# Kernel tuning notes

Measured on AMD Instinct MI355X. Metric: run time of the kernel, lower is better.

Reference implementation:

```python
import jax, jax.numpy as jnp
import numpy as np

GROUPS = 32
EPS = 1e-5


def _group_norm(x, scale, bias):
    B, C, H, W = x.shape
    xg = x.reshape(B, GROUPS, -1)
    mu = xg.mean(axis=-1, keepdims=True)
    var = jnp.mean(jnp.square(xg - mu), axis=-1, keepdims=True)
    xn = ((xg - mu) * jax.lax.rsqrt(var + EPS)).reshape(B, C, H, W)
    return xn * scale[None, :, None, None] + bias[None, :, None, None]


def _conv1x1(x, w, b):
    # x: [B,C,H,W], w: [O,C], b: [O]
    return jnp.einsum('bchw,oc->bohw', x, w) + b[None, :, None, None]


def setup_inputs() -> dict:
    key = jax.random.key(0)
    ks = jax.random.split(key, 6)
    B, C, H, W = 16, 512, 32, 32
    x = jax.random.normal(ks[0], (B, C, H, W), dtype=jnp.float32)
    # xavier_uniform for [C, C, 1, 1] conv: limit = sqrt(6 / (fan_in + fan_out)) = sqrt(6 / (2C))
    lim = float(np.sqrt(6.0 / (2 * C)))
    wq = jax.random.uniform(ks[1], (C, C), jnp.float32, -lim, lim)
    wk = jax.random.uniform(ks[2], (C, C), jnp.float32, -lim, lim)
    wv = jax.random.uniform(ks[3], (C, C), jnp.float32, -lim, lim)
    wo = jax.random.uniform(ks[4], (C, C), jnp.float32, -lim, lim) * 1e-5  # gain=1e-5
    zeros_c = jnp.zeros((C,), jnp.float32)
    return {
        'x': x,
        'gn_scale': jnp.ones((C,), jnp.float32),
        'gn_bias': zeros_c,
        'wq': wq, 'bq': zeros_c,
        'wk': wk, 'bk': zeros_c,
        'wv': wv, 'bv': zeros_c,
        'wo': wo, 'bo': zeros_c,
    }


def reference(x, gn_scale, gn_bias, wq, bq, wk, bk, wv, bv, wo, bo):
    B, C, H, W = x.shape
    N = H * W
    h = _group_norm(x, gn_scale, gn_bias)
    q = _conv1x1(h, wq, bq).reshape(B, C, N)  # [B,C,N]
    k = _conv1x1(h, wk, bk).reshape(B, C, N)
    v = _conv1x1(h, wv, bv).reshape(B, C, N)
    scale = 1.0 / jnp.sqrt(jnp.asarray(C, x.dtype))
    w = jnp.einsum('bcn,bcm->bnm', q, k) * scale  # [B,N,N]
    w = jax.nn.softmax(w, axis=-1)
    hv = jnp.einsum('bnm,bcm->bcn', w, v).reshape(B, C, H, W)
    out = _conv1x1(hv, wo, bo)
    return x + out
```

## Files before the change

### kernel.cpp

```cpp
#include <hip/hip_runtime.h>
#include <hip/hip_bf16.h>
#include <cstdint>

typedef unsigned char u8;
typedef float floatx4 __attribute__((ext_vector_type(4)));
typedef int intx8 __attribute__((ext_vector_type(8)));

__device__ __forceinline__ void gld_lds16(const void* g, void* l) {
    __builtin_amdgcn_global_load_lds(
        (const __attribute__((address_space(1))) unsigned int*)g,
        (__attribute__((address_space(3))) unsigned int*)l, 16, 0, 0);
}

__device__ __forceinline__ u8 f2fp8(float v) {
    return (u8)(__builtin_amdgcn_cvt_pk_fp8_f32(v, v, 0, false) & 0xff);
}
__device__ __forceinline__ unsigned int pack4_fp8(float a, float b, float c, float d) {
    unsigned int u = __builtin_amdgcn_cvt_pk_fp8_f32(a, b, 0, false);
    u = __builtin_amdgcn_cvt_pk_fp8_f32(c, d, u, true);
    return u;
}

__device__ __forceinline__ intx8 ld_frag(const u8* p, int lo, int hi) {
    uint4 a = *(const uint4*)(p + lo);
    uint4 b = *(const uint4*)(p + hi);
    intx8 r;
    r[0] = a.x; r[1] = a.y; r[2] = a.z; r[3] = a.w;
    r[4] = b.x; r[5] = b.y; r[6] = b.z; r[7] = b.w;
    return r;
}
__device__ __forceinline__ intx8 ld_frag_g(const u8* p) {
    uint4 a = *(const uint4*)(p);
    uint4 b = *(const uint4*)(p + 16);
    intx8 r;
    r[0] = a.x; r[1] = a.y; r[2] = a.z; r[3] = a.w;
    r[4] = b.x; r[5] = b.y; r[6] = b.z; r[7] = b.w;
    return r;
}

__global__ __launch_bounds__(256) void setup_kernel(
    const float* __restrict__ x, const float* __restrict__ gs,
    const float* __restrict__ gb,
    const float* __restrict__ wq, const float* __restrict__ wk,
    const float* __restrict__ wv, const float* __restrict__ wo,
    const float* __restrict__ bq, const float* __restrict__ bk,
    const float* __restrict__ bv,
    u8* __restrict__ hT, u8* __restrict__ wqkv, u8* __restrict__ wob,
    float* __restrict__ bqkv, float* __restrict__ lsum)
{
    const int t = threadIdx.x;
    if (blockIdx.x >= 512) {
        int i = (blockIdx.x - 512) * 256 + t;
        if (i < 786432) {
            int which = i >> 18;
            int off = i & 262143;
            const float* src = which == 0 ? wq : which == 1 ? wk : wv;
            wqkv[i] = f2fp8(src[off]);
        } else {
            wob[i - 786432] = f2fp8(wo[i - 786432] * 262144.0f);
        }
        if (i < 1536)
            bqkv[i] = i < 512 ? bq[i] : (i < 1024 ? bk[i - 512] : bv[i - 1024]);
        if (i < 16384)
            lsum[i] = 0.0f;
        return;
    }
    const int b = blockIdx.x >> 5;
    const int g = blockIdx.x & 31;
    const int wave = t >> 6, lane = t & 63;
    const float4* x4 = (const float4*)(x + ((long long)b * 512 + g * 16) * 1024);

    float4 v[16];
    float s1 = 0.f, s2 = 0.f;
#pragma unroll
    for (int i = 0; i < 16; ++i) {
        v[i] = x4[i * 256 + t];
        s1 += v[i].x + v[i].y + v[i].z + v[i].w;
        s2 += v[i].x * v[i].x + v[i].y * v[i].y + v[i].z * v[i].z + v[i].w * v[i].w;
    }
#pragma unroll
    for (int m = 32; m; m >>= 1) {
        s1 += __shfl_xor(s1, m, 64);
        s2 += __shfl_xor(s2, m, 64);
    }
    __shared__ float red[2][4];
    __shared__ float stats[2];
    if (lane == 0) { red[0][wave] = s1; red[1][wave] = s2; }
    __syncthreads();
    if (t == 0) {
        float a = red[0][0] + red[0][1] + red[0][2] + red[0][3];
        float q = red[1][0] + red[1][1] + red[1][2] + red[1][3];
        float mu = a * (1.0f / 16384.0f);
        float var = q * (1.0f / 16384.0f) - mu * mu;
        stats[0] = mu;
        stats[1] = rsqrtf(var + 1e-5f);
    }
    __syncthreads();
    const float mu = stats[0], rs = stats[1];

#pragma unroll
    for (int i = 0; i < 16; ++i) {
        const float sc = gs[g * 16 + i] * rs;
        const float bi = gb[g * 16 + i] - mu * sc;
        v[i].x = v[i].x * sc + bi;
        v[i].y = v[i].y * sc + bi;
        v[i].z = v[i].z * sc + bi;
        v[i].w = v[i].w * sc + bi;
    }
    u8* hb = hT + (long long)b * 524288 + g * 16;
#pragma unroll
    for (int r = 0; r < 4; ++r) {
        uint4 o;
        o.x = pack4_fp8(v[0][r],  v[1][r],  v[2][r],  v[3][r]);
        o.y = pack4_fp8(v[4][r],  v[5][r],  v[6][r],  v[7][r]);
        o.z = pack4_fp8(v[8][r],  v[9][r],  v[10][r], v[11][r]);
        o.w = pack4_fp8(v[12][r], v[13][r], v[14][r], v[15][r]);
        *(uint4*)(hb + (long long)(4 * t + r) * 512) = o;
    }
}

template <int EPI>
__global__ __launch_bounds__(256, 3) void gemm_mx(
    const u8* __restrict__ A, long long sA,
    const u8* __restrict__ B, long long sB,
    void* __restrict__ C, long long sC,
    void* __restrict__ C2, void* __restrict__ C3,
    int ldC, int K,
    const float* __restrict__ bias,
    const float* __restrict__ resid, long long sR,
    float scale, float* __restrict__ lsum)
{
    __shared__ __align__(16) u8 smem[33792];
    const int tid = threadIdx.x;
    const int l = tid & 63;
    const int wave = tid >> 6;
    const int wm = wave >> 1, wn = wave & 1;
    const int bm = blockIdx.x, bn = blockIdx.y, b = blockIdx.z;

    const u8* Ab = A + (long long)b * sA + (long long)bm * 128 * K;
    const u8* Bb = B + (long long)b * sB + (long long)bn * 128 * K;

    const int srow = wave * 8 + (l >> 3);
    const int sg = ((l & 7) ^ ((l >> 3) & 7)) * 16;
    const u8* ga  = Ab + (long long)srow * K + sg;
    const u8* gbp = Bb + (long long)srow * K + sg;
    const long long c32 = (long long)32 * K;
    const int ldst = wave * 1024;

    const int q4 = l >> 4;
    const int glo = ((2 * q4) ^ (l & 7)) * 16;
    const int ghi = ((2 * q4 + 1) ^ (l & 7)) * 16;
    int arow[4], brow[4];
#pragma unroll
    for (int i = 0; i < 4; ++i) {
        arow[i] = (wm * 64 + i * 16 + (l & 15)) * 128;
        brow[i] = (wn * 64 + i * 16 + (l & 15)) * 128 + 16384;
    }

    floatx4 acc[4][4] = {};
    const int niter = K >> 7;

    for (int it = 0; it < niter; ++it) {
        const int k0 = it << 7;
#pragma unroll
        for (int c = 0; c < 4; ++c) {
            gld_lds16(ga + c * c32 + k0, smem + c * 4096 + ldst);
            gld_lds16(gbp + c * c32 + k0, smem + 16384 + c * 4096 + ldst);
        }
        __syncthreads();
        intx8 bfr[4];
#pragma unroll
        for (int j = 0; j < 4; ++j) bfr[j] = ld_frag(smem + brow[j], glo, ghi);
#pragma unroll
        for (int i = 0; i < 4; ++i) {
            intx8 af = ld_frag(smem + arow[i], glo, ghi);
#pragma unroll
            for (int j = 0; j < 4; ++j)
                acc[i][j] = __builtin_amdgcn_mfma_scale_f32_16x16x128_f8f6f4(
                    af, bfr[j], acc[i][j], 0, 0, 0, 127, 0, 127);
        }
        __syncthreads();
    }

    if (EPI == 3) {
        float* Cf = (float*)C;
#pragma unroll
        for (int i = 0; i < 4; ++i) {
            const int mrow = bm * 128 + wm * 64 + i * 16 + q4 * 4;
#pragma unroll
            for (int j = 0; j < 4; ++j) {
                const int ncol = bn * 128 + wn * 64 + j * 16 + (l & 15);
#pragma unroll
                for (int r = 0; r < 4; ++r) {
                    const int row = mrow + r;
                    float v = acc[i][j][r] * scale + bias[row] +
                              resid[(long long)b * sR + (long long)row * ldC + ncol];
                    Cf[(long long)b * sC + (long long)row * ldC + ncol] = v;
                }
            }
        }
    } else if (EPI == 1) {
        const int which = bn >> 2;
        u8* tile = smem;
#pragma unroll
        for (int i = 0; i < 4; ++i) {
            const int rl = wm * 64 + i * 16 + q4 * 4;
#pragma unroll
            for (int j = 0; j < 4; ++j) {
                const int cl = wn * 64 + j * 16 + (l & 15);
                const float badd = bias[bn * 128 + cl];
                if (which == 2) {
                    *(unsigned int*)(tile + cl * 144 + rl) =
                        pack4_fp8(acc[i][j][0] + badd, acc[i][j][1] + badd,
                                  acc[i][j][2] + badd, acc[i][j][3] + badd);
                } else {
#pragma unroll
                    for (int r = 0; r < 4; ++r)
                        tile[(rl + r) * 144 + cl] = f2fp8(acc[i][j][r] + badd);
                }
            }
        }
        __syncthreads();
        const int slot = (tid & 7) * 16;
#pragma unroll
        for (int p = 0; p < 4; ++p) {
            const int row = p * 32 + (tid >> 3);
            uint4 d = *(const uint4*)(tile + row * 144 + slot);
            u8* dst;
            if (which == 0)
                dst = (u8*)C + (long long)b * sC + (long long)(bm * 128 + row) * 512
                      + (bn & 3) * 128 + slot;
            else if (which == 1)
                dst = (u8*)C2 + (long long)b * sC + (long long)(bm * 128 + row) * 512
                      + (bn & 3) * 128 + slot;
            else
                dst = (u8*)C3 + (long long)b * sC + (long long)((bn & 3) * 128 + row) * 1024
                      + bm * 128 + slot;
            *(uint4*)dst = d;
        }
    }
}

__global__ __launch_bounds__(256, 2) void attn_core(
    const u8* __restrict__ qg, const u8* __restrict__ kg,
    const u8* __restrict__ vg, u8* __restrict__ hvT)
{
    __shared__ __align__(16) u8 smem[8704];
    const int tid = threadIdx.x;
    const int l = tid & 63;
    const int w = tid >> 6;
    const int d = blockIdx.x;
    const int b  = (d & 7) * 2 + ((d >> 8) & 1);
    const int bq = (d >> 3) & 31;

    const u8* qb = qg + (long long)b * 524288 + (long long)bq * 32 * 512;
    const u8* kb = kg + (long long)b * 524288;
    const u8* vb = vg + (long long)b * 524288;

    const int q4 = l >> 4;
    const int ln = l & 15;
    const int glo = ((2 * q4) ^ (l & 7)) * 16;
    const int ghi = ((2 * q4 + 1) ^ (l & 7)) * 16;

    intx8 qf[2][4];
#pragma unroll
    for (int j = 0; j < 2; ++j) {
        const u8* qr = qb + (long long)(j * 16 + ln) * 512 + q4 * 32;
#pragma unroll
        for (int kc = 0; kc < 4; ++kc)
            qf[j][kc] = ld_frag_g(qr + kc * 128);
    }

    floatx4 acc_pv[8][2] = {};
    float psum[2] = {0.f, 0.f};
    const float scale = 0.044194173824159216f;

    for (int mt = 0; mt < 8; ++mt) {
        u8* E = smem + (mt & 1) * 4096;
        floatx4 acc_s[2][2] = {};
#pragma unroll
        for (int kc = 0; kc < 4; ++kc) {
#pragma unroll
            for (int i = 0; i < 2; ++i) {
                intx8 kf = ld_frag_g(
                    kb + (long long)(mt * 128 + w * 32 + i * 16 + ln) * 512
                       + kc * 128 + q4 * 32);
#pragma unroll
                for (int j = 0; j < 2; ++j)
                    acc_s[i][j] = __builtin_amdgcn_mfma_scale_f32_16x16x128_f8f6f4(
                        kf, qf[j][kc], acc_s[i][j], 0, 0, 0, 127, 0, 127);
            }
        }
        intx8 vfA[4], vfB[4];
        const u8* vrow = vb + (long long)(w * 128 + ln) * 1024 + mt * 128 + q4 * 32;
#pragma unroll
        for (int i = 0; i < 4; ++i)
            vfA[i] = ld_frag_g(vrow + (long long)i * 16 * 1024);
#pragma unroll
        for (int i = 0; i < 2; ++i) {
#pragma unroll
            for (int j = 0; j < 2; ++j) {
                float e0 = __expf(acc_s[i][j][0] * scale);
                float e1 = __expf(acc_s[i][j][1] * scale);
                float e2 = __expf(acc_s[i][j][2] * scale);
                float e3 = __expf(acc_s[i][j][3] * scale);
                psum[j] += e0 + e1 + e2 + e3;
                const int n = j * 16 + ln;
                const int m0 = w * 32 + i * 16 + q4 * 4;
                *(unsigned int*)(E + n * 128 + (m0 ^ ((n & 7) * 16))) =
                    pack4_fp8(e0 * 0.25f, e1 * 0.25f, e2 * 0.25f, e3 * 0.25f);
            }
        }
        __syncthreads();
#pragma unroll
        for (int i = 0; i < 4; ++i)
            vfB[i] = ld_frag_g(vrow + (long long)(i + 4) * 16 * 1024);
        intx8 ef[2];
#pragma unroll
        for (int j = 0; j < 2; ++j)
            ef[j] = ld_frag(E + (j * 16 + ln) * 128, glo, ghi);
#pragma unroll
        for (int i = 0; i < 4; ++i)
#pragma unroll
            for (int j = 0; j < 2; ++j)
                acc_pv[i][j] = __builtin_amdgcn_mfma_scale_f32_16x16x128_f8f6f4(
                    vfA[i], ef[j], acc_pv[i][j], 0, 0, 0, 127, 0, 127);
#pragma unroll
        for (int i = 0; i < 4; ++i)
#pragma unroll
            for (int j = 0; j < 2; ++j)
                acc_pv[i + 4][j] = __builtin_amdgcn_mfma_scale_f32_16x16x128_f8f6f4(
                    vfB[i], ef[j], acc_pv[i + 4][j], 0, 0, 0, 127, 0, 127);
    }

#pragma unroll
    for (int j = 0; j < 2; ++j) {
        psum[j] += __shfl_xor(psum[j], 16, 64);
        psum[j] += __shfl_xor(psum[j], 32, 64);
    }
    float* sb = (float*)(smem + 8192);
    if (l < 16) {
        sb[w * 32 + l]      = psum[0];
        sb[w * 32 + 16 + l] = psum[1];
    }
    __syncthreads();
    float rln[2];
#pragma unroll
    for (int j = 0; j < 2; ++j) {
        const int n = j * 16 + ln;
        rln[j] = 4.0f / (sb[n] + sb[32 + n] + sb[64 + n] + sb[96 + n]);
    }
    u8* ob = hvT + (long long)b * 524288 + (long long)(bq * 32) * 512;
#pragma unroll
    for (int i = 0; i < 8; ++i) {
#pragma unroll
        for (int j = 0; j < 2; ++j) {
            const int n = j * 16 + ln;
            const int c = w * 128 + i * 16 + q4 * 4;
            *(unsigned int*)(ob + (long long)n * 512 + c) =
                pack4_fp8(acc_pv[i][j][0] * rln[j], acc_pv[i][j][1] * rln[j],
                          acc_pv[i][j][2] * rln[j], acc_pv[i][j][3] * rln[j]);
        }
    }
}

extern "C" void kernel_launch(void* const* d_in, const int* in_sizes, int n_in,
                              void* d_out, int out_size, void* d_ws, size_t ws_size,
                              hipStream_t stream)
{
    const float* x  = (const float*)d_in[0];
    const float* gs = (const float*)d_in[1];
    const float* gb = (const float*)d_in[2];
    const float* wq = (const float*)d_in[3];
    const float* bq = (const float*)d_in[4];
    const float* wk = (const float*)d_in[5];
    const float* bk = (const float*)d_in[6];
    const float* wv = (const float*)d_in[7];
    const float* bv = (const float*)d_in[8];
    const float* wo = (const float*)d_in[9];
    const float* bo = (const float*)d_in[10];
    float* out = (float*)d_out;

    u8* p = (u8*)d_ws;
    u8* hT   = p; p += 8388608;
    u8* q    = p; p += 8388608;
    u8* k    = p; p += 8388608;
    u8* v    = p; p += 8388608;
    u8* wqkv = p; p += 786432;
    float* bqkv = (float*)p; p += 6144;
    u8* wob  = p; p += 262144;
    u8* P    = p; p += 16777216;
    u8* hvT  = p; p += 8388608;
    float* lsum = (float*)p; p += 65536;
    (void)P;

    setup_kernel<<<4608, 256, 0, stream>>>(x, gs, gb, wq, wk, wv, wo, bq, bk, bv,
                                           hT, wqkv, wob, bqkv, lsum);

    gemm_mx<1><<<dim3(8, 12, 16), 256, 0, stream>>>(
        hT, 524288LL, wqkv, 0LL, q, 524288LL, k, v,
        512, 512, bqkv, nullptr, 0LL, 1.0f, nullptr);

    attn_core<<<dim3(512, 1, 1), 256, 0, stream>>>(q, k, v, hvT);

    gemm_mx<3><<<dim3(4, 8, 16), 256, 0, stream>>>(
        wob, 0LL, hvT, 524288LL, out, 524288LL, nullptr, nullptr,
        1024, 512, bo, x, 524288LL, 3.814697265625e-06f, nullptr);
}
```

Measured before the change: 202.8 us.

## Store Q/K/V in MFMA-fragment-tiled layout for contiguous attention loads

The QKV projection epilogue now writes Q, K and V in a tiled layout where each 16-row by 32-byte MFMA fragment block is contiguous. The attention kernel's Q, K and V fragment loads are re-indexed to match. A wave's global loads then cover contiguous 512-byte chunks instead of 32-byte pieces strided across rows, which is meant to cut memory transactions and improve cache-line use. The producer's LDS read pattern and its global store addresses change to fit the new layout.

```diff
diff --git a/kernel.cpp b/kernel.cpp
--- a/kernel.cpp
+++ b/kernel.cpp
@@ -37,6 +37,7 @@
     r[4] = b.x; r[5] = b.y; r[6] = b.z; r[7] = b.w;
     return r;
 }
+
 
 __global__ __launch_bounds__(256) void setup_kernel(
     const float* __restrict__ x, const float* __restrict__ gs,
@@ -221,22 +222,25 @@
             }
         }
         __syncthreads();
-        const int slot = (tid & 7) * 16;
+        const int w2  = wave >> 1;
+        const int cbl = (wave & 1) * 2 + (l >> 5);
+        const int lnw = (l >> 1) & 15;
+        const int g16 = (l & 1) * 16;
 #pragma unroll
         for (int p = 0; p < 4; ++p) {
-            const int row = p * 32 + (tid >> 3);
-            uint4 d = *(const uint4*)(tile + row * 144 + slot);
+            const int rtile = p * 2 + w2;
+            uint4 dd = *(const uint4*)(tile + (rtile * 16 + lnw) * 144 + cbl * 32 + g16);
             u8* dst;
             if (which == 0)
-                dst = (u8*)C + (long long)b * sC + (long long)(bm * 128 + row) * 512
-                      + (bn & 3) * 128 + slot;
+                dst = (u8*)C + (long long)b * sC + (long long)(bm * 8 + rtile) * 8192
+                      + ((bn & 3) * 4 + cbl) * 512 + lnw * 32 + g16;
             else if (which == 1)
-                dst = (u8*)C2 + (long long)b * sC + (long long)(bm * 128 + row) * 512
-                      + (bn & 3) * 128 + slot;
+                dst = (u8*)C2 + (long long)b * sC + (long long)(bm * 8 + rtile) * 8192
+                      + ((bn & 3) * 4 + cbl) * 512 + lnw * 32 + g16;
             else
-                dst = (u8*)C3 + (long long)b * sC + (long long)((bn & 3) * 128 + row) * 1024
-                      + bm * 128 + slot;
-            *(uint4*)dst = d;
+                dst = (u8*)C3 + (long long)b * sC + (long long)((bn & 3) * 8 + rtile) * 16384
+                      + (long long)(bm * 4 + cbl) * 512 + lnw * 32 + g16;
+            *(uint4*)dst = dd;
         }
     }
 }
@@ -253,7 +257,7 @@
     const int b  = (d & 7) * 2 + ((d >> 8) & 1);
     const int bq = (d >> 3) & 31;
 
-    const u8* qb = qg + (long long)b * 524288 + (long long)bq * 32 * 512;
+    const u8* qb = qg + (long long)b * 524288 + (long long)(bq * 2) * 8192;
     const u8* kb = kg + (long long)b * 524288;
     const u8* vb = vg + (long long)b * 524288;
 
@@ -261,15 +265,14 @@
     const int ln = l & 15;
     const int glo = ((2 * q4) ^ (l & 7)) * 16;
     const int ghi = ((2 * q4 + 1) ^ (l & 7)) * 16;
+    const int lo32 = ln * 32;
 
     intx8 qf[2][4];
 #pragma unroll
-    for (int j = 0; j < 2; ++j) {
-        const u8* qr = qb + (long long)(j * 16 + ln) * 512 + q4 * 32;
+    for (int j = 0; j < 2; ++j)
 #pragma unroll
         for (int kc = 0; kc < 4; ++kc)
-            qf[j][kc] = ld_frag_g(qr + kc * 128);
-    }
+            qf[j][kc] = ld_frag_g(qb + j * 8192 + (kc * 4 + q4) * 512 + lo32);
 
     floatx4 acc_pv[8][2] = {};
     float psum[2] = {0.f, 0.f};
@@ -282,9 +285,8 @@
         for (int kc = 0; kc < 4; ++kc) {
 #pragma unroll
             for (int i = 0; i < 2; ++i) {
-                intx8 kf = ld_frag_g(
-                    kb + (long long)(mt * 128 + w * 32 + i * 16 + ln) * 512
-                       + kc * 128 + q4 * 32);
+                intx8 kf = ld_frag_g(kb + (long long)(mt * 8 + w * 2 + i) * 8192
+                                        + (kc * 4 + q4) * 512 + lo32);
 #pragma unroll
                 for (int j = 0; j < 2; ++j)
                     acc_s[i][j] = __builtin_amdgcn_mfma_scale_f32_16x16x128_f8f6f4(
@@ -292,10 +294,10 @@
             }
         }
         intx8 vfA[4], vfB[4];
-        const u8* vrow = vb + (long long)(w * 128 + ln) * 1024 + mt * 128 + q4 * 32;
+        const u8* vrow = vb + (long long)(w * 8) * 16384 + (mt * 4 + q4) * 512 + lo32;
 #pragma unroll
         for (int i = 0; i < 4; ++i)
-            vfA[i] = ld_frag_g(vrow + (long long)i * 16 * 1024);
+            vfA[i] = ld_frag_g(vrow + (long long)i * 16384);
 #pragma unroll
         for (int i = 0; i < 2; ++i) {
 #pragma unroll
@@ -314,7 +316,7 @@
         __syncthreads();
 #pragma unroll
         for (int i = 0; i < 4; ++i)
-            vfB[i] = ld_frag_g(vrow + (long long)(i + 4) * 16 * 1024);
+            vfB[i] = ld_frag_g(vrow + (long long)(i + 4) * 16384);
         intx8 ef[2];
 #pragma unroll
         for (int j = 0; j < 2; ++j)
```

New measurement: 175.2 us. 1.16x faster.
